# Kernel optimization log

Measured on AMD Instinct MI355X. Metric: run time of the kernel, lower is better.

The kernel has to match this reference:

```python
import jax, jax.numpy as jnp
import numpy as np

B, T, D_MODEL, HEAD_DIM = 16, 4096, 512, 64


def setup_inputs() -> dict:
    key = jax.random.key(0)
    kx, kq, kk, kv = jax.random.split(key, 4)
    x = jax.random.normal(kx, (B, T, D_MODEL), dtype=jnp.float32)
    # torch nn.Linear weights, stored pre-transposed as [in, out] for x @ W
    s = 1.0 / np.sqrt(D_MODEL)
    Wq = jax.random.uniform(kq, (D_MODEL, HEAD_DIM), jnp.float32, -s, s)
    Wk = jax.random.uniform(kk, (D_MODEL, HEAD_DIM), jnp.float32, -s, s)
    Wv = jax.random.uniform(kv, (D_MODEL, HEAD_DIM), jnp.float32, -s, s)
    return {"x": x, "Wq": Wq, "Wk": Wk, "Wv": Wv}


def reference(x, Wq, Wk, Wv):
    # Single-head causal self-attention (dropout in eval mode = identity)
    q = x @ Wq  # [B, T, h]
    k = x @ Wk
    v = x @ Wv
    scale = 1.0 / np.sqrt(HEAD_DIM).astype(np.float32)
    scores = jnp.einsum("bth,bsh->bts", q, k) * scale  # [B, T, T]
    t = scores.shape[1]
    causal = jnp.tril(jnp.ones((t, t), dtype=bool))
    scores = jnp.where(causal, scores, -jnp.inf)
    weights = jax.nn.softmax(scores, axis=-1)
    return jnp.einsum("bts,bsh->bth", weights, v)  # [B, T, h]
```

## Files before the change

kernel.cpp:

```cpp
#include <hip/hip_runtime.h>
#include <hip/hip_bf16.h>
#include <math.h>


#define NB 16
#define NT 4096
#define DMODEL 512
#define HD 64
#define CEXP 0.18033688011112042f

typedef unsigned short u16;
typedef unsigned int u32;
typedef __attribute__((ext_vector_type(2))) unsigned int u32x2;
typedef __attribute__((ext_vector_type(8))) short bf16x8;
typedef __attribute__((ext_vector_type(4))) float f32x4;
typedef __attribute__((ext_vector_type(16))) float f32x16;

__device__ __forceinline__ u16 f2bf(float x) {
  union { float f; unsigned u; } v; v.f = x;
  unsigned r = v.u + 0x7fffu + ((v.u >> 16) & 1u);
  return (u16)(r >> 16);
}

__device__ __forceinline__ u32 cvtpk(float lo, float hi) {
  u32 r;
  asm("v_cvt_pk_bf16_f32 %0, %1, %2" : "=v"(r) : "v"(lo), "v"(hi));
  return r;
}

__device__ __forceinline__ u32x2 lane_swap(u32 a, u32 b) {
  asm("v_permlane32_swap_b32 %0, %1" : "+v"(a), "+v"(b));
  u32x2 r; r[0] = a; r[1] = b; return r;
}

__device__ __forceinline__ void gload16(const void* g, void* l) {
  __builtin_amdgcn_global_load_lds(
      (const __attribute__((address_space(1))) void*)g,
      (__attribute__((address_space(3))) void*)l, 16, 0, 0);
}

#define MFMA32(a, b, c) __builtin_amdgcn_mfma_f32_16x16x32_bf16(a, b, c, 0, 0, 0)
#define WMFMA(a, b, c)  __builtin_amdgcn_mfma_f32_32x32x16_bf16(a, b, c, 0, 0, 0)
#define LD8(p) (*(const bf16x8*)(p))

__global__ void prep_wt(const float* __restrict__ Wq, const float* __restrict__ Wk,
                        const float* __restrict__ Wv, u16* __restrict__ Wt) {
  int k0 = blockIdx.x * 16;
  int t = threadIdx.x;
#pragma unroll
  for (int i = 0; i < 12; ++i) {
    int idx = t + i * 256;
    int n = idx % 192;
    int kk = idx / 192;
    const float* W = (n < 64) ? Wq : (n < 128) ? Wk : Wv;
    float w = W[(size_t)(k0 + kk) * 64 + (n & 63)];
    Wt[(size_t)n * 512 + k0 + kk] = f2bf(w);
  }
}

__global__ __launch_bounds__(512) void proj_qkv(const float* __restrict__ x,
                                                const u16* __restrict__ Wt,
                                                u16* __restrict__ qo,
                                                u16* __restrict__ ko,
                                                u16* __restrict__ vo) {
  __shared__ u16 As[128][48];
  int t = threadIdx.x;
  int m0 = blockIdx.x * 128;
  int lane = t & 63, wid = t >> 6;
  int wr = wid >> 2, wc = wid & 3;
  int g = lane >> 4, li = lane & 15;
  f32x4 acc[4][3];
#pragma unroll
  for (int i = 0; i < 4; ++i)
#pragma unroll
    for (int j = 0; j < 3; ++j) acc[i][j] = (f32x4){0.f, 0.f, 0.f, 0.f};

  int row = t >> 2, quad = t & 3;
  for (int k0 = 0; k0 < 512; k0 += 32) {
    __syncthreads();
    const float* src = x + (size_t)(m0 + row) * DMODEL + k0 + quad * 8;
    float4 f0 = *(const float4*)src;
    float4 f1 = *(const float4*)(src + 4);
    union { u16 s[8]; bf16x8 v; } tmp;
    tmp.s[0] = f2bf(f0.x); tmp.s[1] = f2bf(f0.y);
    tmp.s[2] = f2bf(f0.z); tmp.s[3] = f2bf(f0.w);
    tmp.s[4] = f2bf(f1.x); tmp.s[5] = f2bf(f1.y);
    tmp.s[6] = f2bf(f1.z); tmp.s[7] = f2bf(f1.w);
    *(bf16x8*)&As[row][quad * 8] = tmp.v;
    __syncthreads();

    bf16x8 a[4], bb[3];
#pragma unroll
    for (int mf = 0; mf < 4; ++mf)
      a[mf] = *(const bf16x8*)&As[wr * 64 + mf * 16 + li][g * 8];
#pragma unroll
    for (int nf = 0; nf < 3; ++nf)
      bb[nf] = *(const bf16x8*)(Wt + (size_t)(wc * 48 + nf * 16 + li) * 512 + k0 + g * 8);
#pragma unroll
    for (int mf = 0; mf < 4; ++mf)
#pragma unroll
      for (int nf = 0; nf < 3; ++nf)
        acc[mf][nf] = MFMA32(a[mf], bb[nf], acc[mf][nf]);
  }

#pragma unroll
  for (int nf = 0; nf < 3; ++nf) {
    int n = wc * 48 + nf * 16 + li;
    if (n < 64) {
      int col = n;
#pragma unroll
      for (int mf = 0; mf < 4; ++mf)
#pragma unroll
        for (int r = 0; r < 4; ++r) {
          int m = m0 + wr * 64 + mf * 16 + 4 * g + r;
          qo[(size_t)m * HD + col] = f2bf(acc[mf][nf][r] * CEXP);
        }
    } else if (n < 128) {
      int col = n & 63;
      int dt = col >> 4, hh = (col >> 3) & 1, jj = col & 7;
      size_t fo = (size_t)(dt * 2 + hh) * 256 + jj;
#pragma unroll
      for (int mf = 0; mf < 4; ++mf)
#pragma unroll
        for (int r = 0; r < 4; ++r) {
          int m = m0 + wr * 64 + mf * 16 + 4 * g + r;
          ko[(size_t)(m >> 5) * 2048 + fo + (m & 31) * 8] = f2bf(acc[mf][nf][r]);
        }
    } else {
      int d = n - 128;
      int dh = d >> 5, l31d = d & 31;
#pragma unroll
      for (int mf = 0; mf < 4; ++mf) {
        int mbase = m0 + wr * 64 + mf * 16 + 4 * g;
        int kk2 = mbase & 31;
        int kt2 = kk2 >> 4, hh = (kk2 >> 3) & 1;
        size_t off = (size_t)(mbase >> 5) * 2048 +
                     (size_t)((dh * 2 + kt2) * 2 + hh) * 256 + l31d * 8 + (mbase & 7);
        ushort4 pk;
        pk.x = f2bf(acc[mf][nf][0]);
        pk.y = f2bf(acc[mf][nf][1]);
        pk.z = f2bf(acc[mf][nf][2]);
        pk.w = f2bf(acc[mf][nf][3]);
        *(ushort4*)(vo + off) = pk;
      }
    }
  }
}

__global__ __launch_bounds__(256, 4) void attn_fwd9(const u16* __restrict__ qg,
                                                    const u16* __restrict__ kg,
                                                    const u16* __restrict__ vg,
                                                    float* __restrict__ out) {
  __shared__ __align__(16) char smem[33792];
  u16* KV = (u16*)smem;
  float* MrgF = (float*)smem;

  int tid = threadIdx.x;
  int lane = tid & 63, w = tid >> 6;
  int l31 = lane & 31, h = lane >> 5;

  int f = blockIdx.x;
  int xcd = f & 7, i = f >> 3;
  int b, bp;
  if (i < 32) { b = 2 * xcd;     bp = 31 - i; }
  else        { b = 2 * xcd + 1; bp = i - 32; }

  const int limw = 4 * bp + w;
  const int nr = 2 * bp + 2;
  const int q0w = bp * 128 + w * 32;

  const u16* qb = qg + (size_t)b * NT * HD;
  const u16* kbs = kg + (size_t)b * NT * HD;
  const u16* vbs = vg + (size_t)b * NT * HD;
  float* ob = out + (size_t)b * NT * HD;

  bf16x8 qf[4];
#pragma unroll
  for (int dt = 0; dt < 4; ++dt)
    qf[dt] = LD8(qb + (size_t)(q0w + l31) * HD + dt * 16 + 8 * h);

  f32x16 oacc0, oacc1;
#pragma unroll
  for (int r = 0; r < 16; ++r) { oacc0[r] = 0.f; oacc1[r] = 0.f; }
  float lsum = 0.f;

  auto COMPUTE = [&](const u16* kp0, const u16* vp0, int j) {
    bf16x8 kf[4], vf[4];
#pragma unroll
    for (int dt = 0; dt < 4; ++dt)
      kf[dt] = LD8(kp0 + dt * 512 + h * 256 + l31 * 8);
#pragma unroll
    for (int dv = 0; dv < 4; ++dv)
      vf[dv] = LD8(vp0 + dv * 512 + h * 256 + l31 * 8);

    f32x16 sv;
#pragma unroll
    for (int r = 0; r < 16; ++r) sv[r] = 0.f;
    sv = WMFMA(kf[0], qf[0], sv);
    sv = WMFMA(kf[1], qf[1], sv);
    sv = WMFMA(kf[2], qf[2], sv);
    sv = WMFMA(kf[3], qf[3], sv);

    if (j == limw) {
#pragma unroll
      for (int r = 0; r < 16; ++r) {
        int key = (r & 3) + 8 * (r >> 2) + 4 * h;
        if (key > l31) sv[r] = -1e30f;
      }
    }

    float p[16];
#pragma unroll
    for (int r = 0; r < 16; ++r) p[r] = __builtin_amdgcn_exp2f(sv[r]);
    lsum += (((p[0] + p[1]) + (p[2] + p[3])) + ((p[4] + p[5]) + (p[6] + p[7]))) +
            (((p[8] + p[9]) + (p[10] + p[11])) + ((p[12] + p[13]) + (p[14] + p[15])));
    u32 A0 = cvtpk(p[0], p[1]),   A1 = cvtpk(p[2], p[3]);
    u32 B0 = cvtpk(p[4], p[5]),   B1 = cvtpk(p[6], p[7]);
    u32 C0 = cvtpk(p[8], p[9]),   C1 = cvtpk(p[10], p[11]);
    u32 E0 = cvtpk(p[12], p[13]), E1 = cvtpk(p[14], p[15]);
    u32x2 s0 = lane_swap(A0, B0), s1 = lane_swap(A1, B1);
    u32x2 s2 = lane_swap(C0, E0), s3 = lane_swap(C1, E1);
    union { u32 d[4]; bf16x8 v; } f0u, f1u;
    f0u.d[0] = s0[0]; f0u.d[1] = s1[0]; f0u.d[2] = s0[1]; f0u.d[3] = s1[1];
    f1u.d[0] = s2[0]; f1u.d[1] = s3[0]; f1u.d[2] = s2[1]; f1u.d[3] = s3[1];

    oacc0 = WMFMA(vf[0], f0u.v, oacc0);
    oacc1 = WMFMA(vf[2], f0u.v, oacc1);
    oacc0 = WMFMA(vf[1], f1u.v, oacc0);
    oacc1 = WMFMA(vf[3], f1u.v, oacc1);
  };

  gload16(kbs + tid * 8,        KV + tid * 8);
  gload16(vbs + tid * 8,        KV + 2048 + tid * 8);
  gload16(kbs + 2048 + tid * 8, KV + 4096 + tid * 8);
  gload16(vbs + 2048 + tid * 8, KV + 6144 + tid * 8);

  int cur = 0;
  for (int jr = 0; jr < nr; ++jr) {
    if (jr + 1 < nr) {
      const u16* gk = kbs + (size_t)(2 * jr + 2) * 2048 + tid * 8;
      const u16* gv = vbs + (size_t)(2 * jr + 2) * 2048 + tid * 8;
      u16* lb = KV + (cur ^ 1) * 8192;
      gload16(gk,        lb + tid * 8);
      gload16(gv,        lb + 2048 + tid * 8);
      gload16(gk + 2048, lb + 4096 + tid * 8);
      gload16(gv + 2048, lb + 6144 + tid * 8);
      asm volatile("s_waitcnt vmcnt(4)" ::: "memory");
    } else {
      asm volatile("s_waitcnt vmcnt(0)" ::: "memory");
    }
    __builtin_amdgcn_sched_barrier(0);
    asm volatile("s_barrier" ::: "memory");

    const u16* kv0 = KV + cur * 8192;
    int jA = 2 * jr, jB = 2 * jr + 1;
    if (jA <= limw) COMPUTE(kv0, kv0 + 2048, jA);
    if (jB <= limw) COMPUTE(kv0 + 4096, kv0 + 6144, jB);

    asm volatile("s_barrier" ::: "memory");
    cur ^= 1;
  }

  lsum += __shfl_xor(lsum, 32);
  float inv = 1.0f / lsum;
#pragma unroll
  for (int r = 0; r < 16; ++r) { oacc0[r] *= inv; oacc1[r] *= inv; }

  {
    float* mg = MrgF + ((size_t)w * 64 + lane) * 33;
#pragma unroll
    for (int r = 0; r < 16; ++r) { mg[r] = oacc0[r]; mg[16 + r] = oacc1[r]; }
  }
  __syncthreads();
#pragma unroll
  for (int s = 0; s < 8; ++s) {
    int ql = (lane >> 2) + 16 * (s & 1);
    int dq = (lane & 3) + 4 * (s >> 1);
    f32x4 o4;
#pragma unroll
    for (int dd = 0; dd < 4; ++dd) {
      int d = dq * 4 + dd;
      int dh = d >> 5, rem = d & 31;
      int srch = (rem >> 2) & 1;
      int reg = (rem & 3) + ((rem >> 3) << 2);
      o4[dd] = MrgF[((size_t)w * 64 + ql + 32 * srch) * 33 + dh * 16 + reg];
    }
    *(f32x4*)(ob + (size_t)(q0w + ql) * HD + dq * 4) = o4;
  }
}

extern "C" void kernel_launch(void* const* d_in, const int* in_sizes, int n_in,
                              void* d_out, int out_size, void* d_ws, size_t ws_size,
                              hipStream_t stream) {
  const float* x  = (const float*)d_in[0];
  const float* Wq = (const float*)d_in[1];
  const float* Wk = (const float*)d_in[2];
  const float* Wv = (const float*)d_in[3];
  float* out = (float*)d_out;

  u16* Wt  = (u16*)d_ws;
  u16* qws = (u16*)((char*)d_ws + 192 * 512 * 2);
  u16* kws = qws + (size_t)NB * NT * HD;
  u16* vws = kws + (size_t)NB * NT * HD;

  prep_wt<<<32, 256, 0, stream>>>(Wq, Wk, Wv, Wt);
  proj_qkv<<<(NB * NT) / 128, 512, 0, stream>>>(x, Wt, qws, kws, vws);
  attn_fwd9<<<512, 256, 0, stream>>>(qws, kws, vws, out);
}
```

Baseline: 99.14 us.

## Split key range across warp pairs and merge partial sums in LDS

Each block now covers 64 queries instead of 128, with four warps arranged as two query groups by two key-parity halves. Each warp accumulates an unnormalized partial output and row sum over alternating key tiles. The partials are then merged through shared memory before normalization. The grid doubles to 1024 blocks to improve load balance and occupancy across the causal triangle. The cost is the extra merge reads, and each block now loads K/V into LDS for only 64 queries, so global K/V traffic per query doubles.

```diff
diff --git a/kernel.cpp b/kernel.cpp
--- a/kernel.cpp
+++ b/kernel.cpp
@@ -147,10 +147,10 @@
   }
 }
 
-__global__ __launch_bounds__(256, 4) void attn_fwd9(const u16* __restrict__ qg,
-                                                    const u16* __restrict__ kg,
-                                                    const u16* __restrict__ vg,
-                                                    float* __restrict__ out) {
+__global__ __launch_bounds__(256, 4) void attn_fwd10(const u16* __restrict__ qg,
+                                                     const u16* __restrict__ kg,
+                                                     const u16* __restrict__ vg,
+                                                     float* __restrict__ out) {
   __shared__ __align__(16) char smem[33792];
   u16* KV = (u16*)smem;
   float* MrgF = (float*)smem;
@@ -158,16 +158,20 @@
   int tid = threadIdx.x;
   int lane = tid & 63, w = tid >> 6;
   int l31 = lane & 31, h = lane >> 5;
+  int qi = w >> 1, ki = w & 1;
 
   int f = blockIdx.x;
   int xcd = f & 7, i = f >> 3;
+  int m = i >> 5, cu = i & 31;
   int b, bp;
-  if (i < 32) { b = 2 * xcd;     bp = 31 - i; }
-  else        { b = 2 * xcd + 1; bp = i - 32; }
-
-  const int limw = 4 * bp + w;
-  const int nr = 2 * bp + 2;
-  const int q0w = bp * 128 + w * 32;
+  if (m == 0)      { b = 2 * xcd;     bp = 63 - cu; }
+  else if (m == 1) { b = 2 * xcd;     bp = 31 - cu; }
+  else if (m == 2) { b = 2 * xcd + 1; bp = cu;      }
+  else             { b = 2 * xcd + 1; bp = 32 + cu; }
+
+  const int diag = 2 * bp + qi;
+  const int nr = bp + 1;
+  const int q0w = bp * 64 + qi * 32;
 
   const u16* qb = qg + (size_t)b * NT * HD;
   const u16* kbs = kg + (size_t)b * NT * HD;
@@ -184,7 +188,7 @@
   for (int r = 0; r < 16; ++r) { oacc0[r] = 0.f; oacc1[r] = 0.f; }
   float lsum = 0.f;
 
-  auto COMPUTE = [&](const u16* kp0, const u16* vp0, int j) {
+  auto COMPUTE = [&](const u16* kp0, const u16* vp0, bool maskdiag) {
     bf16x8 kf[4], vf[4];
 #pragma unroll
     for (int dt = 0; dt < 4; ++dt)
@@ -201,7 +205,7 @@
     sv = WMFMA(kf[2], qf[2], sv);
     sv = WMFMA(kf[3], qf[3], sv);
 
-    if (j == limw) {
+    if (maskdiag) {
 #pragma unroll
       for (int r = 0; r < 16; ++r) {
         int key = (r & 3) + 8 * (r >> 2) + 4 * h;
@@ -253,37 +257,39 @@
     asm volatile("s_barrier" ::: "memory");
 
     const u16* kv0 = KV + cur * 8192;
-    int jA = 2 * jr, jB = 2 * jr + 1;
-    if (jA <= limw) COMPUTE(kv0, kv0 + 2048, jA);
-    if (jB <= limw) COMPUTE(kv0 + 4096, kv0 + 6144, jB);
+    int jmine = 2 * jr + ki;
+    if (jmine <= diag)
+      COMPUTE(kv0 + ki * 4096, kv0 + ki * 4096 + 2048, jmine == diag);
 
     asm volatile("s_barrier" ::: "memory");
     cur ^= 1;
   }
 
   lsum += __shfl_xor(lsum, 32);
-  float inv = 1.0f / lsum;
-#pragma unroll
-  for (int r = 0; r < 16; ++r) { oacc0[r] *= inv; oacc1[r] *= inv; }
-
   {
     float* mg = MrgF + ((size_t)w * 64 + lane) * 33;
 #pragma unroll
     for (int r = 0; r < 16; ++r) { mg[r] = oacc0[r]; mg[16 + r] = oacc1[r]; }
+    mg[32] = lsum;
   }
   __syncthreads();
 #pragma unroll
-  for (int s = 0; s < 8; ++s) {
+  for (int s = 0; s < 4; ++s) {
     int ql = (lane >> 2) + 16 * (s & 1);
-    int dq = (lane & 3) + 4 * (s >> 1);
+    int dq = ki * 8 + (lane & 3) + 4 * (s >> 1);
+    const float* m0p = MrgF + ((size_t)(qi * 2) * 64) * 33;
+    const float* m1p = MrgF + ((size_t)(qi * 2 + 1) * 64) * 33;
+    float ls = m0p[(size_t)ql * 33 + 32] + m1p[(size_t)ql * 33 + 32];
+    float inv = 1.0f / ls;
     f32x4 o4;
 #pragma unroll
     for (int dd = 0; dd < 4; ++dd) {
       int d = dq * 4 + dd;
       int dh = d >> 5, rem = d & 31;
       int srch = (rem >> 2) & 1;
-      int reg = (rem & 3) + ((rem >> 3) << 2);
-      o4[dd] = MrgF[((size_t)w * 64 + ql + 32 * srch) * 33 + dh * 16 + reg];
+      int reg = dh * 16 + (rem & 3) + ((rem >> 3) << 2);
+      size_t ro = (size_t)(ql + 32 * srch) * 33 + reg;
+      o4[dd] = (m0p[ro] + m1p[ro]) * inv;
     }
     *(f32x4*)(ob + (size_t)(q0w + ql) * HD + dq * 4) = o4;
   }
@@ -305,5 +311,5 @@
 
   prep_wt<<<32, 256, 0, stream>>>(Wq, Wk, Wv, Wt);
   proj_qkv<<<(NB * NT) / 128, 512, 0, stream>>>(x, Wt, qws, kws, vws);
-  attn_fwd9<<<512, 256, 0, stream>>>(qws, kws, vws, out);
-}
+  attn_fwd10<<<1024, 256, 0, stream>>>(qws, kws, vws, out);
+}
```

After: 96.75 us. 1.02x faster.
